# Performance work log

Measured on AMD Instinct MI355X. Metric: run time of the kernel, lower is better.

## Reference

```python
import math
import jax, jax.numpy as jnp
import numpy as np

BS, Q_LEN, DIM = 8, 16, 4096
MAX_SEQ = 4096
N_Q_HEADS, N_KV_HEADS, HEAD_DIM = 32, 8, 128
REP = N_Q_HEADS // N_KV_HEADS


def setup_inputs() -> dict:
    key = jax.random.key(0)
    ks = jax.random.split(key, 12)
    w = 0.02
    return {
        "x": jax.random.normal(ks[0], (BS, Q_LEN, DIM), jnp.float32),
        "k_cache": jax.random.normal(ks[1], (BS, MAX_SEQ, N_KV_HEADS, HEAD_DIM), jnp.float32),
        "v_cache": jax.random.normal(ks[2], (BS, MAX_SEQ, N_KV_HEADS, HEAD_DIM), jnp.float32),
        "Wq": jax.random.normal(ks[3], (DIM, N_Q_HEADS * HEAD_DIM), jnp.float32) * w,
        "bq": jax.random.normal(ks[4], (N_Q_HEADS * HEAD_DIM,), jnp.float32) * w,
        "Wk": jax.random.normal(ks[5], (DIM, N_KV_HEADS * HEAD_DIM), jnp.float32) * w,
        "bk": jax.random.normal(ks[6], (N_KV_HEADS * HEAD_DIM,), jnp.float32) * w,
        "Wv": jax.random.normal(ks[7], (DIM, N_KV_HEADS * HEAD_DIM), jnp.float32) * w,
        "bv": jax.random.normal(ks[8], (N_KV_HEADS * HEAD_DIM,), jnp.float32) * w,
        "Wo": jax.random.normal(ks[9], (N_Q_HEADS * HEAD_DIM, DIM), jnp.float32) * w,
        "bo": jax.random.normal(ks[10], (DIM,), jnp.float32) * w,
        "start_pos": MAX_SEQ - Q_LEN,
        "seq_len_for_kv": Q_LEN,
    }


def reference(x, k_cache, v_cache, Wq, bq, Wk, bk, Wv, bv, Wo, bo, start_pos, seq_len_for_kv):
    bs, sl, dim = x.shape
    # Projections (torch Linear: x @ W^T + b; here W stored as [in, out])
    q = (x @ Wq + bq).reshape(bs, sl, N_KV_HEADS, REP, HEAD_DIM)  # [b, q, g, r, d]
    k = (x @ Wk + bk).reshape(bs, sl, N_KV_HEADS, HEAD_DIM)
    v = (x @ Wv + bv).reshape(bs, sl, N_KV_HEADS, HEAD_DIM)
    # KV-cache append (start_pos / seq_len_for_kv are static Python ints)
    k_cache = k_cache.at[:, start_pos:start_pos + seq_len_for_kv].set(k)
    v_cache = v_cache.at[:, start_pos:start_pos + seq_len_for_kv].set(v)
    kv_len = start_pos + seq_len_for_kv
    keys = k_cache[:, :kv_len]    # [b, L, g, d]
    vals = v_cache[:, :kv_len]    # [b, L, g, d]
    # GQA: each kv head g serves REP query heads r (broadcast instead of repeat_kv)
    scale = 1.0 / math.sqrt(HEAD_DIM)
    scores = jnp.einsum('bqgrd,blgd->bgrql', q, keys) * scale  # [b, g, r, q, L]
    att = jax.nn.softmax(scores, axis=-1)
    out = jnp.einsum('bgrql,blgd->bqgrd', att, vals)           # [b, q, g, r, d]
    out = out.reshape(bs, sl, N_Q_HEADS * HEAD_DIM)
    return out @ Wo + bo
```

## Files before the change

kernel.cpp:

```cpp
#include <hip/hip_runtime.h>
#include <math.h>

#define DIM       4096
#define NKVH      8
#define HD        128
#define MAX_SEQ   4096
#define START_POS 4080
#define NQKV      6144
#define NCHUNK    8
#define CHUNK     512
#define KS        8
#define ATT_SCALE 0.08838834764831845f

#define WS_PART   0
#define WS_QH     6291456
#define WS_QL     6553600
#define WS_KNEW   6815744
#define WS_VNEW   6946816
#define WS_PM     7077888
#define WS_PL     7110656
#define WS_ATH    7143424
#define WS_ATL    7405568
#define WS_XH     7667712
#define WS_XL     7929856
#define WS_PARTO  WS_PART

typedef __bf16 bf16x8 __attribute__((ext_vector_type(8)));
typedef float  f32x4  __attribute__((ext_vector_type(4)));
typedef unsigned int uintx4 __attribute__((ext_vector_type(4)));

__device__ __forceinline__ unsigned short f2bf(float f) {
    return __builtin_bit_cast(unsigned short, (__bf16)f);
}
__device__ __forceinline__ float bf2f(unsigned short h) {
    union { unsigned int u; float f; } v; v.u = ((unsigned int)h) << 16;
    return v.f;
}
__device__ __forceinline__ void splitbf(float f, unsigned short &h, unsigned short &l) {
    h = f2bf(f);
    l = f2bf(f - bf2f(h));
}
__device__ __forceinline__ bf16x8 ldsfrag(const unsigned short* p) {
    uintx4 u = *(const uintx4*)p;
    return __builtin_bit_cast(bf16x8, u);
}
__device__ __forceinline__ bf16x8 ldsfrag2(const unsigned short* p) {
    union { uint2 u2[2]; bf16x8 v; } u;
    u.u2[0] = *(const uint2*)p;
    u.u2[1] = *(const uint2*)(p + 4);
    return u.v;
}
#define MFMA16(a,b,c) __builtin_amdgcn_mfma_f32_16x16x32_bf16(a, b, c, 0, 0, 0)
#define VCOMP(v,j) ((j)==0?(v).x:((j)==1?(v).y:((j)==2?(v).z:(v).w)))

__global__ __launch_bounds__(256) void split_x_kernel(
    const float* __restrict__ x, unsigned short* __restrict__ xh,
    unsigned short* __restrict__ xl, int n4)
{
    int i = blockIdx.x * 256 + threadIdx.x;
    if (i < n4) {
        float4 v = *(const float4*)(x + (size_t)i * 4);
        ushort4 h, l;
        splitbf(v.x, h.x, l.x);
        splitbf(v.y, h.y, l.y);
        splitbf(v.z, h.z, l.z);
        splitbf(v.w, h.w, l.w);
        *(ushort4*)(xh + (size_t)i * 4) = h;
        *(ushort4*)(xl + (size_t)i * 4) = l;
    }
}

__device__ __forceinline__ void gemm_body(
    const unsigned short* __restrict__ Ah, const unsigned short* __restrict__ Al,
    const float* __restrict__ W, int ldW, int noff,
    float* __restrict__ part, int partStride, int ncol0, int ks,
    unsigned short* Ahs, unsigned short* Als, unsigned short* Bs)
{
    const int t = threadIdx.x;
    const int w = t >> 6, lane = t & 63, l15 = lane & 15, quad = lane >> 4;
    f32x4 acc[2][4];
    #pragma unroll
    for (int i = 0; i < 2; ++i)
        #pragma unroll
        for (int nt = 0; nt < 4; ++nt) acc[i][nt] = (f32x4){0.f, 0.f, 0.f, 0.f};

    const int k0base = ks * 512;
    uintx4 areg_h[4], areg_l[4];
    float4 wreg[4];

    auto LOAD = [&](int it) {
        int k0 = k0base + it * 64;
        #pragma unroll
        for (int i = 0; i < 4; ++i) {
            int f = t + i * 256;
            int row = f >> 3, c0 = (f & 7) << 3;
            size_t off = (size_t)row * DIM + k0 + c0;
            areg_h[i] = *(const uintx4*)(Ah + off);
            areg_l[i] = *(const uintx4*)(Al + off);
        }
        #pragma unroll
        for (int i = 0; i < 4; ++i) {
            int kk = (t >> 4) + 16 * i;
            int n0 = (t & 15) << 2;
            wreg[i] = *(const float4*)(W + (size_t)(k0 + kk) * ldW + noff + n0);
        }
    };

    LOAD(0);
    for (int it = 0; it < 8; ++it) {
        __syncthreads();
        #pragma unroll
        for (int i = 0; i < 4; ++i) {
            int f = t + i * 256;
            int row = f >> 3, c0 = (f & 7) << 3;
            *(uintx4*)(Ahs + row * 72 + c0) = areg_h[i];
            *(uintx4*)(Als + row * 72 + c0) = areg_l[i];
        }
        {
            int n0 = (t & 15) << 2;
            #pragma unroll
            for (int i = 0; i < 4; ++i) {
                int kk = (t >> 4) + 16 * i;
                #pragma unroll
                for (int j = 0; j < 4; ++j)
                    Bs[(n0 + j) * 68 + kk] = f2bf(VCOMP(wreg[i], j));
            }
        }
        __syncthreads();
        if (it < 7) LOAD(it + 1);
        #pragma unroll
        for (int kt = 0; kt < 2; ++kt) {
            int ko = kt * 32 + quad * 8;
            bf16x8 ah0 = ldsfrag(Ahs + ((2*w+0)*16 + l15) * 72 + ko);
            bf16x8 ah1 = ldsfrag(Ahs + ((2*w+1)*16 + l15) * 72 + ko);
            bf16x8 al0 = ldsfrag(Als + ((2*w+0)*16 + l15) * 72 + ko);
            bf16x8 al1 = ldsfrag(Als + ((2*w+1)*16 + l15) * 72 + ko);
            #pragma unroll
            for (int nt = 0; nt < 4; ++nt) {
                bf16x8 b = ldsfrag2(Bs + (nt*16 + l15) * 68 + ko);
                acc[0][nt] = MFMA16(ah0, b, acc[0][nt]);
                acc[0][nt] = MFMA16(al0, b, acc[0][nt]);
                acc[1][nt] = MFMA16(ah1, b, acc[1][nt]);
                acc[1][nt] = MFMA16(al1, b, acc[1][nt]);
            }
        }
    }
    #pragma unroll
    for (int i = 0; i < 2; ++i)
        #pragma unroll
        for (int nt = 0; nt < 4; ++nt)
            #pragma unroll
            for (int r = 0; r < 4; ++r) {
                int row = (2*w + i) * 16 + quad * 4 + r;
                int col = ncol0 + nt * 16 + l15;
                part[(size_t)(ks * 128 + row) * partStride + col] = acc[i][nt][r];
            }
}

__global__ __launch_bounds__(256) void qkv_gemm_kernel(
    const unsigned short* __restrict__ xh, const unsigned short* __restrict__ xl,
    const float* __restrict__ Wq, const float* __restrict__ Wk,
    const float* __restrict__ Wv, float* __restrict__ part)
{
    __shared__ unsigned short Ahs[128 * 72], Als[128 * 72];
    __shared__ unsigned short Bs[64 * 68];
    int ncol0 = blockIdx.x * 64;
    int ks = blockIdx.y;
    const float* W; int ldW, noff;
    if (ncol0 < 4096)      { W = Wq; ldW = 4096; noff = ncol0; }
    else if (ncol0 < 5120) { W = Wk; ldW = 1024; noff = ncol0 - 4096; }
    else                   { W = Wv; ldW = 1024; noff = ncol0 - 5120; }
    gemm_body(xh, xl, W, ldW, noff, part, NQKV, ncol0, ks, Ahs, Als, Bs);
}

__global__ __launch_bounds__(256) void oproj_gemm_kernel(
    const unsigned short* __restrict__ ah, const unsigned short* __restrict__ al,
    const float* __restrict__ Wo, float* __restrict__ part)
{
    __shared__ unsigned short Ahs[128 * 72], Als[128 * 72];
    __shared__ unsigned short Bs[64 * 68];
    int ncol0 = blockIdx.x * 64;
    int ks = blockIdx.y;
    gemm_body(ah, al, Wo, 4096, ncol0, part, 4096, ncol0, ks, Ahs, Als, Bs);
}

__global__ __launch_bounds__(256) void qkv_reduce_kernel(
    const float* __restrict__ part, const float* __restrict__ bq,
    const float* __restrict__ bk, const float* __restrict__ bv,
    unsigned short* __restrict__ qh, unsigned short* __restrict__ ql,
    float* __restrict__ k_new, float* __restrict__ v_new)
{
    int gid = blockIdx.x * 256 + threadIdx.x;
    int row = gid / 1536;
    int c4  = gid - row * 1536;
    int n = c4 * 4;
    float4 s = make_float4(0.f, 0.f, 0.f, 0.f);
    #pragma unroll
    for (int j = 0; j < KS; ++j) {
        float4 p = *(const float4*)&part[(size_t)(j * 128 + row) * NQKV + n];
        s.x += p.x; s.y += p.y; s.z += p.z; s.w += p.w;
    }
    if (n < 4096) {
        float4 b4 = *(const float4*)&bq[n];
        ushort4 h, l;
        splitbf(s.x + b4.x, h.x, l.x);
        splitbf(s.y + b4.y, h.y, l.y);
        splitbf(s.z + b4.z, h.z, l.z);
        splitbf(s.w + b4.w, h.w, l.w);
        *(ushort4*)&qh[row * 4096 + n] = h;
        *(ushort4*)&ql[row * 4096 + n] = l;
    } else if (n < 5120) {
        float4 b4 = *(const float4*)&bk[n - 4096];
        float4 o = make_float4(s.x + b4.x, s.y + b4.y, s.z + b4.z, s.w + b4.w);
        *(float4*)&k_new[row * 1024 + (n - 4096)] = o;
    } else {
        float4 b4 = *(const float4*)&bv[n - 5120];
        float4 o = make_float4(s.x + b4.x, s.y + b4.y, s.z + b4.z, s.w + b4.w);
        *(float4*)&v_new[row * 1024 + (n - 5120)] = o;
    }
}

__global__ __launch_bounds__(512, 2) void attn_partial7_kernel(
    const unsigned short* __restrict__ qhp, const unsigned short* __restrict__ qlp,
    const float* __restrict__ kc, const float* __restrict__ vc,
    const float* __restrict__ knew, const float* __restrict__ vnew,
    float* __restrict__ part_O, float* __restrict__ part_m, float* __restrict__ part_l)
{
    __shared__ unsigned short Kb[2][64][136];
    __shared__ unsigned short Vt[2][128][76];
    __shared__ unsigned short Pw[8][16 * 76];

    const int t = threadIdx.x;
    const int w = t >> 6, lane = t & 63, l15 = lane & 15, quad = lane >> 4;
    const int gsel = w >> 2;
    const int rep  = w & 3;
    const int blk = blockIdx.x;
    const int b = blk >> 5, gg = (blk >> 3) & 3, c = blk & 7;
    const int g = gg * 2 + gsel;

    const int p0 = t >> 6;
    const int q4 = t & 63;
    const int gl = q4 >> 5;
    const int d0 = (q4 & 31) << 2;

    bf16x8 qhf[4], qlf[4];
    {
        size_t base = (size_t)(b * 16 + l15) * DIM + (g * 4 + rep) * HD + quad * 8;
        #pragma unroll
        for (int kt = 0; kt < 4; ++kt) {
            qhf[kt] = ldsfrag(qhp + base + kt * 32);
            qlf[kt] = ldsfrag(qlp + base + kt * 32);
        }
    }

    float m_run[4], l_run[4];
    f32x4 oacc[8];
    #pragma unroll
    for (int r = 0; r < 4; ++r) { m_run[r] = -INFINITY; l_run[r] = 0.f; }
    #pragma unroll
    for (int d = 0; d < 8; ++d) oacc[d] = (f32x4){0.f, 0.f, 0.f, 0.f};

    float4 kreg[8], vreg[8];
    auto LOADKV = [&](int it) {
        #pragma unroll
        for (int i = 0; i < 8; ++i) {
            int pos = p0 + i * 8;
            int pg = c * CHUNK + it * 64 + pos;
            const float *ksrc, *vsrc;
            if (pg >= START_POS) {
                size_t off = (size_t)(b * 16 + pg - START_POS) * (NKVH * HD) + gg * 256 + q4 * 4;
                ksrc = knew + off; vsrc = vnew + off;
            } else {
                size_t off = ((size_t)(b * MAX_SEQ + pg) * NKVH) * HD + gg * 256 + q4 * 4;
                ksrc = kc + off; vsrc = vc + off;
            }
            kreg[i] = *(const float4*)ksrc;
            vreg[i] = *(const float4*)vsrc;
        }
    };

    unsigned short* phw = Pw[w];
    const int slotbase = (l15 & 7) * 8 + (l15 >> 3);

    LOADKV(0);
    for (int it = 0; it < 8; ++it) {
        __syncthreads();
        #pragma unroll
        for (int i = 0; i < 8; ++i) {
            int pos = p0 + i * 8;
            ushort4 k4 = make_ushort4(f2bf(kreg[i].x), f2bf(kreg[i].y),
                                      f2bf(kreg[i].z), f2bf(kreg[i].w));
            *(ushort4*)&Kb[gl][pos][d0] = k4;
        }
        #pragma unroll
        for (int j = 0; j < 4; ++j) {
            ushort4 vlo = make_ushort4(f2bf(VCOMP(vreg[0], j)), f2bf(VCOMP(vreg[1], j)),
                                       f2bf(VCOMP(vreg[2], j)), f2bf(VCOMP(vreg[3], j)));
            ushort4 vhi = make_ushort4(f2bf(VCOMP(vreg[4], j)), f2bf(VCOMP(vreg[5], j)),
                                       f2bf(VCOMP(vreg[6], j)), f2bf(VCOMP(vreg[7], j)));
            *(ushort4*)&Vt[gl][d0 + j][p0 * 8]     = vlo;
            *(ushort4*)&Vt[gl][d0 + j][p0 * 8 + 4] = vhi;
        }
        __syncthreads();
        if (it + 1 < 8) LOADKV(it + 1);

        f32x4 sacc[4];
        #pragma unroll
        for (int nt = 0; nt < 4; ++nt) sacc[nt] = (f32x4){0.f,0.f,0.f,0.f};
        #pragma unroll
        for (int nt = 0; nt < 4; ++nt)
            #pragma unroll
            for (int kt = 0; kt < 4; ++kt) {
                bf16x8 bh = ldsfrag(&Kb[gsel][nt*16 + l15][kt*32 + quad*8]);
                sacc[nt] = MFMA16(qhf[kt], bh, sacc[nt]);
                sacc[nt] = MFMA16(qlf[kt], bh, sacc[nt]);
            }

        float e0[4], e1[4], e2[4], e3[4], alpha[4];
        #pragma unroll
        for (int r = 0; r < 4; ++r) {
            float s0 = sacc[0][r] * ATT_SCALE;
            float s1 = sacc[1][r] * ATT_SCALE;
            float s2 = sacc[2][r] * ATT_SCALE;
            float s3 = sacc[3][r] * ATT_SCALE;
            float mx = fmaxf(fmaxf(s0, s1), fmaxf(s2, s3));
            mx = fmaxf(mx, __shfl_xor(mx, 1));
            mx = fmaxf(mx, __shfl_xor(mx, 2));
            mx = fmaxf(mx, __shfl_xor(mx, 4));
            mx = fmaxf(mx, __shfl_xor(mx, 8));
            float mnew = fmaxf(m_run[r], mx);
            alpha[r] = __expf(m_run[r] - mnew);
            e0[r] = __expf(s0 - mnew);
            e1[r] = __expf(s1 - mnew);
            e2[r] = __expf(s2 - mnew);
            e3[r] = __expf(s3 - mnew);
            float sum = (e0[r] + e1[r]) + (e2[r] + e3[r]);
            sum += __shfl_xor(sum, 1);
            sum += __shfl_xor(sum, 2);
            sum += __shfl_xor(sum, 4);
            sum += __shfl_xor(sum, 8);
            l_run[r] = l_run[r] * alpha[r] + sum;
            m_run[r] = mnew;
        }
        #pragma unroll
        for (int d = 0; d < 8; ++d)
            #pragma unroll
            for (int r = 0; r < 4; ++r) oacc[d][r] *= alpha[r];

        #pragma unroll
        for (int r = 0; r < 4; ++r) {
            unsigned short* pr = phw + (quad*4 + r) * 76 + slotbase;
            pr[0] = f2bf(e0[r]);
            pr[2] = f2bf(e1[r]);
            pr[4] = f2bf(e2[r]);
            pr[6] = f2bf(e3[r]);
        }
        bf16x8 pa0 = ldsfrag2(phw + l15 * 76 + quad * 8);
        bf16x8 pa1 = ldsfrag2(phw + l15 * 76 + 32 + quad * 8);

        #pragma unroll
        for (int dt = 0; dt < 8; ++dt) {
            bf16x8 vb0 = ldsfrag2(&Vt[gsel][dt*16 + l15][quad * 8]);
            oacc[dt] = MFMA16(pa0, vb0, oacc[dt]);
            bf16x8 vb1 = ldsfrag2(&Vt[gsel][dt*16 + l15][32 + quad * 8]);
            oacc[dt] = MFMA16(pa1, vb1, oacc[dt]);
        }
    }

    const size_t obase = (size_t)((b * 8 + g) * 8 + c) * 64 + rep * 16 + quad * 4;
    #pragma unroll
    for (int dt = 0; dt < 8; ++dt)
        #pragma unroll
        for (int r = 0; r < 4; ++r)
            part_O[(obase + r) * HD + dt * 16 + l15] = oacc[dt][r];
    if (l15 == 0) {
        #pragma unroll
        for (int r = 0; r < 4; ++r) {
            part_m[obase + r] = m_run[r];
            part_l[obase + r] = l_run[r];
        }
    }
}

__global__ __launch_bounds__(128) void attn_combine_kernel(
    const float* __restrict__ part_O, const float* __restrict__ part_m,
    const float* __restrict__ part_l, unsigned short* __restrict__ ah,
    unsigned short* __restrict__ al)
{
    int bid = blockIdx.x;
    int d = threadIdx.x;
    int bg = bid >> 6;
    int row = bid & 63;
    float mc[NCHUNK], lc[NCHUNK];
    float M = -INFINITY;
    #pragma unroll
    for (int cc = 0; cc < NCHUNK; ++cc) {
        mc[cc] = part_m[(bg * NCHUNK + cc) * 64 + row];
        lc[cc] = part_l[(bg * NCHUNK + cc) * 64 + row];
        M = fmaxf(M, mc[cc]);
    }
    float L = 0.f, acc = 0.f;
    #pragma unroll
    for (int cc = 0; cc < NCHUNK; ++cc) {
        float wgt = __expf(mc[cc] - M);
        L += lc[cc] * wgt;
        acc += part_O[((size_t)(bg * NCHUNK + cc) * 64 + row) * HD + d] * wgt;
    }
    int b = bg >> 3, g = bg & 7;
    int r = row >> 4, qp = row & 15;
    float v = acc / L;
    unsigned short h, l; splitbf(v, h, l);
    size_t idx = (size_t)(b * 16 + qp) * DIM + (g * 4 + r) * HD + d;
    ah[idx] = h; al[idx] = l;
}

__global__ __launch_bounds__(256) void oproj_reduce_kernel(
    const float* __restrict__ part, const float* __restrict__ bo,
    float* __restrict__ out)
{
    int gid4 = blockIdx.x * 256 + threadIdx.x;
    int n = (gid4 & 1023) * 4;
    float4 s = make_float4(0.f, 0.f, 0.f, 0.f);
    #pragma unroll
    for (int j = 0; j < KS; ++j) {
        float4 p = *(const float4*)&part[(size_t)j * 524288 + (size_t)gid4 * 4];
        s.x += p.x; s.y += p.y; s.z += p.z; s.w += p.w;
    }
    float4 b4 = *(const float4*)&bo[n];
    float4 o = make_float4(s.x + b4.x, s.y + b4.y, s.z + b4.z, s.w + b4.w);
    *(float4*)&out[(size_t)gid4 * 4] = o;
}

extern "C" void kernel_launch(void* const* d_in, const int* in_sizes, int n_in,
                              void* d_out, int out_size, void* d_ws, size_t ws_size,
                              hipStream_t stream)
{
    const float* x  = (const float*)d_in[0];
    const float* kc = (const float*)d_in[1];
    const float* vc = (const float*)d_in[2];
    const float* Wq = (const float*)d_in[3];
    const float* bq = (const float*)d_in[4];
    const float* Wk = (const float*)d_in[5];
    const float* bk = (const float*)d_in[6];
    const float* Wv = (const float*)d_in[7];
    const float* bv = (const float*)d_in[8];
    const float* Wo = (const float*)d_in[9];
    const float* bo = (const float*)d_in[10];
    float* out = (float*)d_out;
    float* ws  = (float*)d_ws;

    unsigned short* xh = (unsigned short*)(ws + WS_XH);
    unsigned short* xl = (unsigned short*)(ws + WS_XL);
    unsigned short* qh = (unsigned short*)(ws + WS_QH);
    unsigned short* ql = (unsigned short*)(ws + WS_QL);
    unsigned short* ath = (unsigned short*)(ws + WS_ATH);
    unsigned short* atl = (unsigned short*)(ws + WS_ATL);

    split_x_kernel<<<512, 256, 0, stream>>>(x, xh, xl, 131072);
    qkv_gemm_kernel<<<dim3(96, KS), 256, 0, stream>>>(xh, xl, Wq, Wk, Wv, ws + WS_PART);
    qkv_reduce_kernel<<<768, 256, 0, stream>>>(ws + WS_PART, bq, bk, bv,
                                               qh, ql, ws + WS_KNEW, ws + WS_VNEW);
    attn_partial7_kernel<<<256, 512, 0, stream>>>(qh, ql, kc, vc,
                                                  ws + WS_KNEW, ws + WS_VNEW,
                                                  ws + WS_PARTO, ws + WS_PM, ws + WS_PL);
    attn_combine_kernel<<<4096, 128, 0, stream>>>(ws + WS_PARTO, ws + WS_PM,
                                                  ws + WS_PL, ath, atl);
    oproj_gemm_kernel<<<dim3(64, KS), 256, 0, stream>>>(ath, atl, Wo, ws + WS_PART);
    oproj_reduce_kernel<<<512, 256, 0, stream>>>(ws + WS_PART, bo, out);
}
```

Measured before the change: 435.8 us.

## Replace split-K GEMMs plus reduce kernels with direct full-K tiled GEMMs

The QKV and output-projection GEMMs no longer use split-K with partial buffers and separate reduce kernels. Each block now computes a 32x128 output tile over the full K=4096 and applies bias, the bf16 hi/lo split, and the final store in its epilogue. This removes two kernel launches and the write and re-read of large partial-sum buffers. The cost is far fewer blocks (192 and 128 instead of 768 and 512), a longer serial K loop per block, and Wo/W reloaded from global once per M-tile (4x), which may leave the GPU underutilized.

```diff
diff --git a/kernel.cpp b/kernel.cpp
--- a/kernel.cpp
+++ b/kernel.cpp
@@ -9,10 +9,9 @@
 #define NQKV      6144
 #define NCHUNK    8
 #define CHUNK     512
-#define KS        8
 #define ATT_SCALE 0.08838834764831845f
 
-#define WS_PART   0
+#define WS_PARTO  0
 #define WS_QH     6291456
 #define WS_QL     6553600
 #define WS_KNEW   6815744
@@ -23,7 +22,6 @@
 #define WS_ATL    7405568
 #define WS_XH     7667712
 #define WS_XL     7929856
-#define WS_PARTO  WS_PART
 
 typedef __bf16 bf16x8 __attribute__((ext_vector_type(8)));
 typedef float  f32x4  __attribute__((ext_vector_type(4)));
@@ -70,154 +68,126 @@
     }
 }
 
-__device__ __forceinline__ void gemm_body(
+__device__ __forceinline__ void gemm_direct_loop(
     const unsigned short* __restrict__ Ah, const unsigned short* __restrict__ Al,
-    const float* __restrict__ W, int ldW, int noff,
-    float* __restrict__ part, int partStride, int ncol0, int ks,
-    unsigned short* Ahs, unsigned short* Als, unsigned short* Bs)
+    const float* __restrict__ W, int ldW, int noff, int mrow0,
+    unsigned short* Ahs, unsigned short* Als, unsigned short* Bs,
+    f32x4 (&acc)[4])
 {
     const int t = threadIdx.x;
     const int w = t >> 6, lane = t & 63, l15 = lane & 15, quad = lane >> 4;
-    f32x4 acc[2][4];
-    #pragma unroll
-    for (int i = 0; i < 2; ++i)
-        #pragma unroll
-        for (int nt = 0; nt < 4; ++nt) acc[i][nt] = (f32x4){0.f, 0.f, 0.f, 0.f};
-
-    const int k0base = ks * 512;
-    uintx4 areg_h[4], areg_l[4];
-    float4 wreg[4];
-
+    const int wm = w & 1, wn = w >> 1;
+    #pragma unroll
+    for (int nt = 0; nt < 4; ++nt) acc[nt] = (f32x4){0.f, 0.f, 0.f, 0.f};
+
+    const int arow = t >> 3, ac0 = (t & 7) << 3;
+    const int n4 = t & 31, kk = t >> 5;
+
+    uintx4 areg_h, areg_l;
+    float4 wreg[8];
     auto LOAD = [&](int it) {
-        int k0 = k0base + it * 64;
-        #pragma unroll
-        for (int i = 0; i < 4; ++i) {
-            int f = t + i * 256;
-            int row = f >> 3, c0 = (f & 7) << 3;
-            size_t off = (size_t)row * DIM + k0 + c0;
-            areg_h[i] = *(const uintx4*)(Ah + off);
-            areg_l[i] = *(const uintx4*)(Al + off);
-        }
-        #pragma unroll
-        for (int i = 0; i < 4; ++i) {
-            int kk = (t >> 4) + 16 * i;
-            int n0 = (t & 15) << 2;
-            wreg[i] = *(const float4*)(W + (size_t)(k0 + kk) * ldW + noff + n0);
-        }
+        int k0 = it * 64;
+        size_t aoff = (size_t)(mrow0 + arow) * DIM + k0 + ac0;
+        areg_h = *(const uintx4*)(Ah + aoff);
+        areg_l = *(const uintx4*)(Al + aoff);
+        #pragma unroll
+        for (int i = 0; i < 8; ++i)
+            wreg[i] = *(const float4*)(W + (size_t)(k0 + kk + 8 * i) * ldW + noff + n4 * 4);
     };
 
     LOAD(0);
-    for (int it = 0; it < 8; ++it) {
+    for (int it = 0; it < 64; ++it) {
         __syncthreads();
-        #pragma unroll
-        for (int i = 0; i < 4; ++i) {
-            int f = t + i * 256;
-            int row = f >> 3, c0 = (f & 7) << 3;
-            *(uintx4*)(Ahs + row * 72 + c0) = areg_h[i];
-            *(uintx4*)(Als + row * 72 + c0) = areg_l[i];
-        }
-        {
-            int n0 = (t & 15) << 2;
+        *(uintx4*)(Ahs + arow * 72 + ac0) = areg_h;
+        *(uintx4*)(Als + arow * 72 + ac0) = areg_l;
+        #pragma unroll
+        for (int i = 0; i < 8; ++i)
             #pragma unroll
-            for (int i = 0; i < 4; ++i) {
-                int kk = (t >> 4) + 16 * i;
-                #pragma unroll
-                for (int j = 0; j < 4; ++j)
-                    Bs[(n0 + j) * 68 + kk] = f2bf(VCOMP(wreg[i], j));
-            }
-        }
+            for (int j = 0; j < 4; ++j)
+                Bs[(n4 * 4 + j) * 68 + kk + 8 * i] = f2bf(VCOMP(wreg[i], j));
         __syncthreads();
-        if (it < 7) LOAD(it + 1);
+        if (it < 63) LOAD(it + 1);
         #pragma unroll
         for (int kt = 0; kt < 2; ++kt) {
             int ko = kt * 32 + quad * 8;
-            bf16x8 ah0 = ldsfrag(Ahs + ((2*w+0)*16 + l15) * 72 + ko);
-            bf16x8 ah1 = ldsfrag(Ahs + ((2*w+1)*16 + l15) * 72 + ko);
-            bf16x8 al0 = ldsfrag(Als + ((2*w+0)*16 + l15) * 72 + ko);
-            bf16x8 al1 = ldsfrag(Als + ((2*w+1)*16 + l15) * 72 + ko);
+            bf16x8 ah = ldsfrag(Ahs + (wm * 16 + l15) * 72 + ko);
+            bf16x8 al = ldsfrag(Als + (wm * 16 + l15) * 72 + ko);
             #pragma unroll
             for (int nt = 0; nt < 4; ++nt) {
-                bf16x8 b = ldsfrag2(Bs + (nt*16 + l15) * 68 + ko);
-                acc[0][nt] = MFMA16(ah0, b, acc[0][nt]);
-                acc[0][nt] = MFMA16(al0, b, acc[0][nt]);
-                acc[1][nt] = MFMA16(ah1, b, acc[1][nt]);
-                acc[1][nt] = MFMA16(al1, b, acc[1][nt]);
+                bf16x8 b = ldsfrag2(Bs + ((wn * 4 + nt) * 16 + l15) * 68 + ko);
+                acc[nt] = MFMA16(ah, b, acc[nt]);
+                acc[nt] = MFMA16(al, b, acc[nt]);
             }
         }
     }
-    #pragma unroll
-    for (int i = 0; i < 2; ++i)
-        #pragma unroll
-        for (int nt = 0; nt < 4; ++nt)
-            #pragma unroll
-            for (int r = 0; r < 4; ++r) {
-                int row = (2*w + i) * 16 + quad * 4 + r;
-                int col = ncol0 + nt * 16 + l15;
-                part[(size_t)(ks * 128 + row) * partStride + col] = acc[i][nt][r];
-            }
-}
-
-__global__ __launch_bounds__(256) void qkv_gemm_kernel(
+}
+
+__global__ __launch_bounds__(256) void qkv_gemm_direct_kernel(
     const unsigned short* __restrict__ xh, const unsigned short* __restrict__ xl,
     const float* __restrict__ Wq, const float* __restrict__ Wk,
-    const float* __restrict__ Wv, float* __restrict__ part)
-{
-    __shared__ unsigned short Ahs[128 * 72], Als[128 * 72];
-    __shared__ unsigned short Bs[64 * 68];
-    int ncol0 = blockIdx.x * 64;
-    int ks = blockIdx.y;
+    const float* __restrict__ Wv,
+    const float* __restrict__ bq, const float* __restrict__ bk,
+    const float* __restrict__ bv,
+    unsigned short* __restrict__ qh, unsigned short* __restrict__ ql,
+    float* __restrict__ k_new, float* __restrict__ v_new)
+{
+    __shared__ unsigned short Ahs[32 * 72], Als[32 * 72], Bs[128 * 68];
+    int ncol0 = blockIdx.x * 128;
+    int mrow0 = blockIdx.y * 32;
     const float* W; int ldW, noff;
     if (ncol0 < 4096)      { W = Wq; ldW = 4096; noff = ncol0; }
     else if (ncol0 < 5120) { W = Wk; ldW = 1024; noff = ncol0 - 4096; }
     else                   { W = Wv; ldW = 1024; noff = ncol0 - 5120; }
-    gemm_body(xh, xl, W, ldW, noff, part, NQKV, ncol0, ks, Ahs, Als, Bs);
-}
-
-__global__ __launch_bounds__(256) void oproj_gemm_kernel(
+
+    f32x4 acc[4];
+    gemm_direct_loop(xh, xl, W, ldW, noff, mrow0, Ahs, Als, Bs, acc);
+
+    const int t = threadIdx.x;
+    const int w = t >> 6, lane = t & 63, l15 = lane & 15, quad = lane >> 4;
+    const int wm = w & 1, wn = w >> 1;
+    #pragma unroll
+    for (int nt = 0; nt < 4; ++nt)
+        #pragma unroll
+        for (int r = 0; r < 4; ++r) {
+            int row = mrow0 + wm * 16 + quad * 4 + r;
+            int col = ncol0 + (wn * 4 + nt) * 16 + l15;
+            float v = acc[nt][r];
+            if (col < 4096) {
+                float q = v + bq[col];
+                unsigned short h, l; splitbf(q, h, l);
+                qh[row * 4096 + col] = h;
+                ql[row * 4096 + col] = l;
+            } else if (col < 5120) {
+                k_new[row * 1024 + (col - 4096)] = v + bk[col - 4096];
+            } else {
+                v_new[row * 1024 + (col - 5120)] = v + bv[col - 5120];
+            }
+        }
+}
+
+__global__ __launch_bounds__(256) void oproj_gemm_direct_kernel(
     const unsigned short* __restrict__ ah, const unsigned short* __restrict__ al,
-    const float* __restrict__ Wo, float* __restrict__ part)
-{
-    __shared__ unsigned short Ahs[128 * 72], Als[128 * 72];
-    __shared__ unsigned short Bs[64 * 68];
-    int ncol0 = blockIdx.x * 64;
-    int ks = blockIdx.y;
-    gemm_body(ah, al, Wo, 4096, ncol0, part, 4096, ncol0, ks, Ahs, Als, Bs);
-}
-
-__global__ __launch_bounds__(256) void qkv_reduce_kernel(
-    const float* __restrict__ part, const float* __restrict__ bq,
-    const float* __restrict__ bk, const float* __restrict__ bv,
-    unsigned short* __restrict__ qh, unsigned short* __restrict__ ql,
-    float* __restrict__ k_new, float* __restrict__ v_new)
-{
-    int gid = blockIdx.x * 256 + threadIdx.x;
-    int row = gid / 1536;
-    int c4  = gid - row * 1536;
-    int n = c4 * 4;
-    float4 s = make_float4(0.f, 0.f, 0.f, 0.f);
-    #pragma unroll
-    for (int j = 0; j < KS; ++j) {
-        float4 p = *(const float4*)&part[(size_t)(j * 128 + row) * NQKV + n];
-        s.x += p.x; s.y += p.y; s.z += p.z; s.w += p.w;
-    }
-    if (n < 4096) {
-        float4 b4 = *(const float4*)&bq[n];
-        ushort4 h, l;
-        splitbf(s.x + b4.x, h.x, l.x);
-        splitbf(s.y + b4.y, h.y, l.y);
-        splitbf(s.z + b4.z, h.z, l.z);
-        splitbf(s.w + b4.w, h.w, l.w);
-        *(ushort4*)&qh[row * 4096 + n] = h;
-        *(ushort4*)&ql[row * 4096 + n] = l;
-    } else if (n < 5120) {
-        float4 b4 = *(const float4*)&bk[n - 4096];
-        float4 o = make_float4(s.x + b4.x, s.y + b4.y, s.z + b4.z, s.w + b4.w);
-        *(float4*)&k_new[row * 1024 + (n - 4096)] = o;
-    } else {
-        float4 b4 = *(const float4*)&bv[n - 5120];
-        float4 o = make_float4(s.x + b4.x, s.y + b4.y, s.z + b4.z, s.w + b4.w);
-        *(float4*)&v_new[row * 1024 + (n - 5120)] = o;
-    }
+    const float* __restrict__ Wo, const float* __restrict__ bo,
+    float* __restrict__ out)
+{
+    __shared__ unsigned short Ahs[32 * 72], Als[32 * 72], Bs[128 * 68];
+    int ncol0 = blockIdx.x * 128;
+    int mrow0 = blockIdx.y * 32;
+
+    f32x4 acc[4];
+    gemm_direct_loop(ah, al, Wo, 4096, ncol0, mrow0, Ahs, Als, Bs, acc);
+
+    const int t = threadIdx.x;
+    const int w = t >> 6, lane = t & 63, l15 = lane & 15, quad = lane >> 4;
+    const int wm = w & 1, wn = w >> 1;
+    #pragma unroll
+    for (int nt = 0; nt < 4; ++nt)
+        #pragma unroll
+        for (int r = 0; r < 4; ++r) {
+            int row = mrow0 + wm * 16 + quad * 4 + r;
+            int col = ncol0 + (wn * 4 + nt) * 16 + l15;
+            out[(size_t)row * 4096 + col] = acc[nt][r] + bo[col];
+        }
 }
 
 __global__ __launch_bounds__(512, 2) void attn_partial7_kernel(
@@ -414,23 +384,6 @@
     ah[idx] = h; al[idx] = l;
 }
 
-__global__ __launch_bounds__(256) void oproj_reduce_kernel(
-    const float* __restrict__ part, const float* __restrict__ bo,
-    float* __restrict__ out)
-{
-    int gid4 = blockIdx.x * 256 + threadIdx.x;
-    int n = (gid4 & 1023) * 4;
-    float4 s = make_float4(0.f, 0.f, 0.f, 0.f);
-    #pragma unroll
-    for (int j = 0; j < KS; ++j) {
-        float4 p = *(const float4*)&part[(size_t)j * 524288 + (size_t)gid4 * 4];
-        s.x += p.x; s.y += p.y; s.z += p.z; s.w += p.w;
-    }
-    float4 b4 = *(const float4*)&bo[n];
-    float4 o = make_float4(s.x + b4.x, s.y + b4.y, s.z + b4.z, s.w + b4.w);
-    *(float4*)&out[(size_t)gid4 * 4] = o;
-}
-
 extern "C" void kernel_launch(void* const* d_in, const int* in_sizes, int n_in,
                               void* d_out, int out_size, void* d_ws, size_t ws_size,
                               hipStream_t stream)
@@ -457,14 +410,13 @@
     unsigned short* atl = (unsigned short*)(ws + WS_ATL);
 
     split_x_kernel<<<512, 256, 0, stream>>>(x, xh, xl, 131072);
-    qkv_gemm_kernel<<<dim3(96, KS), 256, 0, stream>>>(xh, xl, Wq, Wk, Wv, ws + WS_PART);
-    qkv_reduce_kernel<<<768, 256, 0, stream>>>(ws + WS_PART, bq, bk, bv,
-                                               qh, ql, ws + WS_KNEW, ws + WS_VNEW);
+    qkv_gemm_direct_kernel<<<dim3(48, 4), 256, 0, stream>>>(
+        xh, xl, Wq, Wk, Wv, bq, bk, bv, qh, ql, ws + WS_KNEW, ws + WS_VNEW);
     attn_partial7_kernel<<<256, 512, 0, stream>>>(qh, ql, kc, vc,
                                                   ws + WS_KNEW, ws + WS_VNEW,
                                                   ws + WS_PARTO, ws + WS_PM, ws + WS_PL);
     attn_combine_kernel<<<4096, 128, 0, stream>>>(ws + WS_PARTO, ws + WS_PM,
                                                   ws + WS_PL, ath, atl);
-    oproj_gemm_kernel<<<dim3(64, KS), 256, 0, stream>>>(ath, atl, Wo, ws + WS_PART);
-    oproj_reduce_kernel<<<512, 256, 0, stream>>>(ws + WS_PART, bo, out);
-}
+    oproj_gemm_direct_kernel<<<dim3(32, 4), 256, 0, stream>>>(
+        ath, atl, Wo, bo, out);
+}
```

Measured after the change: 589.2 us. 35.2% more time.
